# Optimization experiments

Hardware: AMD Instinct MI355X
Metric: run time of the kernel (lower is better)

The kernel has to match this reference:

```python
import jax, jax.numpy as jnp
import numpy as np

N_NODES = 50000
N_EDGES = 800000
EPS = 1e-5

def _xavier(key, shape):
    fan_in, fan_out = shape[1], shape[0]
    lim = float(np.sqrt(6.0 / (fan_in + fan_out)))
    return jax.random.uniform(key, shape, jnp.float32, -lim, lim)

def setup_inputs() -> dict:
    key = jax.random.key(0)
    ks = jax.random.split(key, 12)
    x = jax.random.normal(ks[0], (N_NODES, 166), jnp.float32)
    edge_index = jax.random.randint(ks[1], (2, N_EDGES), 0, N_NODES, jnp.int32)
    dims = [(256, 166), (128, 256), (64, 128)]
    inp = {"x": x, "edge_index": edge_index}
    # SAGEConv layers: lin_l (applied to aggregated neighbors, has bias) and lin_r (self)
    names = ["1", "2", "e"]
    for i, (nm, (do, di)) in enumerate(zip(names, dims)):
        inp[f"Wl{nm}"] = _xavier(ks[2 + 2 * i], (do, di))
        inp[f"Wr{nm}"] = _xavier(ks[3 + 2 * i], (do, di))
        inp[f"b{nm}"] = jnp.zeros((do,), jnp.float32)
    # BatchNorm params for the two hidden conv layers
    inp["g1"] = jnp.ones((256,), jnp.float32); inp["bt1"] = jnp.zeros((256,), jnp.float32)
    inp["g2"] = jnp.ones((128,), jnp.float32); inp["bt2"] = jnp.zeros((128,), jnp.float32)
    # classifier
    inp["Wc"] = _xavier(ks[8], (2, 64))
    inp["bc"] = jnp.zeros((2,), jnp.float32)
    return inp

def _sage_conv(x, src, dst, Wl, Wr, b):
    # mean aggregation of source features at destination nodes
    agg = jax.ops.segment_sum(x[src], dst, num_segments=N_NODES)  # [N, d]
    deg = jax.ops.segment_sum(jnp.ones((src.shape[0],), x.dtype), dst, num_segments=N_NODES)
    agg = agg / jnp.maximum(deg, 1.0)[:, None]
    return agg @ Wl.T + x @ Wr.T + b

def _bn(x, g, b):
    m = jnp.mean(x, axis=0)
    v = jnp.var(x, axis=0)
    return (x - m) * jax.lax.rsqrt(v + EPS) * g + b

def reference(x, edge_index, Wl1, Wr1, b1, Wl2, Wr2, b2, Wle, Wre, be, g1, bt1, g2, bt2, Wc, bc):
    src, dst = edge_index[0], edge_index[1]
    h = _sage_conv(x, src, dst, Wl1, Wr1, b1)
    h = jax.nn.relu(_bn(h, g1, bt1))
    h = _sage_conv(h, src, dst, Wl2, Wr2, b2)
    h = jax.nn.relu(_bn(h, g2, bt2))
    embeddings = _sage_conv(h, src, dst, Wle, Wre, be)  # [N, 64]
    logits = embeddings @ Wc.T + bc  # [N, 2]
    return (logits, embeddings)
```

## Files before the change

kernel.cpp:

```cpp
#include <hip/hip_runtime.h>

#define NN 50000
#define NE 800000
#define NB 256
#define BNODES ((NN + NB - 1) / NB)
#define CAP 4096
static constexpr float BN_EPS = 1e-5f;

typedef __attribute__((ext_vector_type(8))) short bf16x8;
typedef __attribute__((ext_vector_type(4))) float f32x4;

__device__ inline unsigned short f2bf(float f) {
  unsigned int u = __float_as_uint(f);
  return (unsigned short)((u + 0x7FFFu + ((u >> 16) & 1u)) >> 16);
}
__device__ inline float bf2f(unsigned int h) { return __uint_as_float(h << 16); }
__device__ inline void gl_lds16(const char* g, char* l) {
  __builtin_amdgcn_global_load_lds((const __attribute__((address_space(1))) void*)g,
                                   (__attribute__((address_space(3))) void*)l, 16, 0, 0);
}

__global__ void k_bpart(const int* __restrict__ src, const int* __restrict__ dst,
                        int* __restrict__ bcur, uint2* __restrict__ pairs) {
  __shared__ int cnt[NB], lbase[NB], lcur[NB];
  int t = threadIdx.x;
  cnt[t] = 0;
  __syncthreads();
  int e0 = blockIdx.x * 8192 + t;
#pragma unroll
  for (int i = 0; i < 32; ++i) {
    int e = e0 + i * 256;
    if (e < NE) atomicAdd(&cnt[dst[e] / BNODES], 1);
  }
  __syncthreads();
  lbase[t] = cnt[t] ? (t * CAP + atomicAdd(&bcur[t], cnt[t])) : 0;
  lcur[t] = 0;
  __syncthreads();
#pragma unroll
  for (int i = 0; i < 32; ++i) {
    int e = e0 + i * 256;
    if (e < NE) {
      int d = dst[e];
      int b = d / BNODES;
      int p = atomicAdd(&lcur[b], 1);
      pairs[(size_t)lbase[b] + p] = uint2{(unsigned)src[e], (unsigned)d};
    }
  }
}

__global__ void k_bscatter(const uint2* __restrict__ pairs, const int* __restrict__ bcur,
                           int2* __restrict__ begend, int* __restrict__ col) {
  __shared__ int dcnt[NB], ts[NB], doff[NB], dcur[NB];
  int t = threadIdx.x;
  int b = blockIdx.x;
  int n0 = b * BNODES;
  int ncnt = min(NN - n0, BNODES);
  int e0 = b * CAP, e1 = e0 + bcur[b];
  dcnt[t] = 0;
  __syncthreads();
  for (int e = e0 + t; e < e1; e += 256) atomicAdd(&dcnt[pairs[e].y - n0], 1);
  __syncthreads();
  ts[t] = dcnt[t];
  __syncthreads();
#pragma unroll
  for (int off = 1; off < NB; off <<= 1) {
    int u = (t >= off) ? ts[t - off] : 0;
    __syncthreads();
    ts[t] += u;
    __syncthreads();
  }
  doff[t] = ts[t] - dcnt[t];
  dcur[t] = 0;
  if (t < ncnt) begend[n0 + t] = int2{e0 + doff[t], e0 + doff[t] + dcnt[t]};
  __syncthreads();
  for (int e = e0 + t; e < e1; e += 256) {
    uint2 pr = pairs[e];
    int ld = pr.y - n0;
    int p = atomicAdd(&dcur[ld], 1);
    col[e0 + doff[ld] + p] = (int)pr.x;
  }
}

__global__ void k_prep_x(const float* __restrict__ x, unsigned int* __restrict__ xbu,
                         unsigned int* __restrict__ X1u) {
  int i = blockIdx.x * 256 + threadIdx.x;
  if (i >= NN * 96) return;
  int r = i / 96, q = i - r * 96;
  if (q < 84) {
    int c0 = 2 * q, c1 = c0 + 1;
    float v0 = (c0 < 166) ? x[(size_t)r * 166 + c0] : 0.f;
    float v1 = (c1 < 166) ? x[(size_t)r * 166 + c1] : 0.f;
    unsigned int u = (unsigned)f2bf(v0) | ((unsigned)f2bf(v1) << 16);
    xbu[(size_t)r * 96 + q] = u;
    X1u[(size_t)r * 192 + 96 + q] = u;
  } else {
    int z = q - 84;
    X1u[(size_t)r * 192 + 84 + z] = 0u;
    X1u[(size_t)r * 192 + 180 + z] = 0u;
    if (z == 0) X1u[(size_t)r * 192 + 83] = 0u;
  }
}

__global__ void k_pack_w_all(const float* __restrict__ Wl1, const float* __restrict__ Wr1,
                             const float* __restrict__ Wl2, const float* __restrict__ Wr2,
                             const float* __restrict__ Wle, const float* __restrict__ Wre,
                             unsigned short* __restrict__ w1c, unsigned short* __restrict__ w2s,
                             unsigned short* __restrict__ w3s) {
  int idx = blockIdx.x * 256 + threadIdx.x;
  if (idx < 98304) {
    int n = idx / 384, k = idx - n * 384;
    float v = 0.f;
    if (k < 166) v = Wl1[(size_t)n * 166 + k];
    else if (k >= 192 && k < 358) v = Wr1[(size_t)n * 166 + (k - 192)];
    w1c[idx] = f2bf(v);
  } else if (idx < 163840) {
    int j = idx - 98304;
    int n = j / 256, k = j - n * 256;
    w2s[j] = f2bf(n < 128 ? Wl2[(size_t)n * 256 + k] : Wr2[(size_t)(n - 128) * 256 + k]);
  } else if (idx < 180224) {
    int j = idx - 163840;
    int n = j / 128, k = j - n * 128;
    w3s[j] = f2bf(n < 64 ? Wle[(size_t)n * 128 + k] : Wre[(size_t)(n - 64) * 128 + k]);
  }
}

template <int D, int U, bool FUSE, bool OUTBF, bool CLS>
__global__ __launch_bounds__(256) void k_aggb(
    const unsigned int* __restrict__ feat, int fsu,
    const int2* __restrict__ begend, const int* __restrict__ col,
    const unsigned int* __restrict__ self, int ssu,
    const float* __restrict__ bias,
    void* __restrict__ outv, int osu,
    const float* __restrict__ Wc, const float* __restrict__ bc,
    float* __restrict__ logits) {
  constexpr int D2 = D / 2;
  constexpr int LPN = (D2 < 64) ? D2 : 64;
  constexpr int NPB = 256 / LPN;
  constexpr int C = (D2 + LPN - 1) / LPN;
  int node = blockIdx.x * NPB + threadIdx.x / LPN;
  if (node >= NN) return;
  int lane = threadIdx.x % LPN;
  int2 be = begend[node];
  int beg = be.x, end = be.y;
  float ax[C], ay[C];
#pragma unroll
  for (int c = 0; c < C; ++c) { ax[c] = 0.f; ay[c] = 0.f; }

  int j = beg;
  for (; j + U <= end; j += U) {
    const unsigned int* fp[U];
#pragma unroll
    for (int u = 0; u < U; ++u) fp[u] = feat + (size_t)col[j + u] * fsu;
#pragma unroll
    for (int c = 0; c < C; ++c) {
      int p = lane + c * LPN;
      unsigned int t[U];
#pragma unroll
      for (int u = 0; u < U; ++u) t[u] = (p < D2) ? fp[u][p] : 0u;
#pragma unroll
      for (int u = 0; u < U; ++u) {
        ax[c] += bf2f(t[u] & 0xffffu);
        ay[c] += bf2f(t[u] >> 16);
      }
    }
  }
  for (; j < end; ++j) {
    const unsigned int* fr = feat + (size_t)col[j] * fsu;
#pragma unroll
    for (int c = 0; c < C; ++c) {
      int p = lane + c * LPN;
      if (p < D2) {
        unsigned int t = fr[p];
        ax[c] += bf2f(t & 0xffffu);
        ay[c] += bf2f(t >> 16);
      }
    }
  }
  float inv = 1.0f / fmaxf((float)(end - beg), 1.0f);
  float s0 = 0.f, s1 = 0.f;
#pragma unroll
  for (int c = 0; c < C; ++c) {
    int p = lane + c * LPN;
    if (p < D2) {
      float vx = ax[c] * inv, vy = ay[c] * inv;
      if constexpr (FUSE) {
        unsigned int s = self[(size_t)node * ssu + p];
        vx += bf2f(s & 0xffffu) + bias[2 * p];
        vy += bf2f(s >> 16) + bias[2 * p + 1];
      }
      if constexpr (OUTBF) {
        unsigned int o = (unsigned int)f2bf(vx) | ((unsigned int)f2bf(vy) << 16);
        ((unsigned int*)outv)[(size_t)node * osu + p] = o;
      } else {
        float2 o{vx, vy};
        *reinterpret_cast<float2*>((float*)outv + (size_t)node * osu + 2 * p) = o;
      }
      if constexpr (CLS) {
        s0 += vx * Wc[2 * p] + vy * Wc[2 * p + 1];
        s1 += vx * Wc[64 + 2 * p] + vy * Wc[64 + 2 * p + 1];
      }
    }
  }
  if constexpr (CLS) {
#pragma unroll
    for (int m = 1; m < LPN; m <<= 1) {
      s0 += __shfl_xor(s0, m);
      s1 += __shfl_xor(s1, m);
    }
    if (lane == 0) {
      logits[node * 2 + 0] = s0 + bc[0];
      logits[node * 2 + 1] = s1 + bc[1];
    }
  }
}

template <bool BIASED, bool STATS>
__global__ __launch_bounds__(256) void k_gemm_mfma(
    const unsigned short* __restrict__ A, int KC,
    const unsigned short* __restrict__ W,
    const float* __restrict__ bias,
    unsigned short* __restrict__ out, int Ntot,
    float* __restrict__ statacc) {
  __shared__ __align__(16) char lds[65536];
  int tid = threadIdx.x;
  int lane = tid & 63;
  int w = tid >> 6;
  int wr = w >> 1, wc = w & 1;
  int m0 = blockIdx.x * 128;
  int n0 = blockIdx.y * 128;

  int srow = lane >> 3;
  int scol = (lane & 7) << 4;
  int ssw = scol ^ (srow << 4);
  const char* Ab = (const char*)A;
  const char* Wb = (const char*)W;

  f32x4 acc[4][4];
#pragma unroll
  for (int i = 0; i < 4; ++i)
#pragma unroll
    for (int j = 0; j < 4; ++j) acc[i][j] = f32x4{0.f, 0.f, 0.f, 0.f};

  auto stage = [&](int buf, int k0) {
    char* dst = lds + buf * 32768 + w * 4096;
#pragma unroll
    for (int i = 0; i < 4; ++i) {
      int row = w * 32 + i * 8 + srow;
      int ga = m0 + row;
      ga = ga < NN ? ga : NN - 1;
      gl_lds16(Ab + ((size_t)ga * KC + k0) * 2 + ssw, dst + i * 1024);
      gl_lds16(Wb + ((size_t)(n0 + row) * KC + k0) * 2 + ssw, dst + 16384 + i * 1024);
    }
  };
  auto compute = [&](int buf) {
    char* lA = lds + buf * 32768;
    char* lB = lA + 16384;
#pragma unroll
    for (int ks = 0; ks < 2; ++ks) {
      bf16x8 af[4], bfr[4];
      int ac = ks * 64 + ((lane >> 4) << 4);
#pragma unroll
      for (int f = 0; f < 4; ++f) {
        int ar = wr * 64 + f * 16 + (lane & 15);
        af[f] = *reinterpret_cast<const bf16x8*>(lA + ar * 128 + (ac ^ ((ar & 7) << 4)));
        int br = wc * 64 + f * 16 + (lane & 15);
        bfr[f] = *reinterpret_cast<const bf16x8*>(lB + br * 128 + (ac ^ ((br & 7) << 4)));
      }
#pragma unroll
      for (int fm = 0; fm < 4; ++fm)
#pragma unroll
        for (int fn = 0; fn < 4; ++fn)
          acc[fm][fn] = __builtin_amdgcn_mfma_f32_16x16x32_bf16(af[fm], bfr[fn], acc[fm][fn], 0, 0, 0);
    }
  };

  int nt = KC >> 6;
  stage(0, 0);
  __syncthreads();
  int cur = 0;
  for (int t = 0; t < nt; ++t) {
    if (t + 1 < nt) stage(cur ^ 1, (t + 1) << 6);
    compute(cur);
    __syncthreads();
    cur ^= 1;
  }

  int nbase = n0 + wc * 64 + (lane & 15);
  float bv[4] = {0.f, 0.f, 0.f, 0.f};
  if constexpr (BIASED) {
#pragma unroll
    for (int fn = 0; fn < 4; ++fn) bv[fn] = bias[nbase + fn * 16];
  }
  float ssum[4] = {0.f, 0.f, 0.f, 0.f}, sqs[4] = {0.f, 0.f, 0.f, 0.f};
#pragma unroll
  for (int fm = 0; fm < 4; ++fm) {
    int mbase = m0 + wr * 64 + fm * 16 + ((lane >> 4) << 2);
#pragma unroll
    for (int j = 0; j < 4; ++j) {
      int m = mbase + j;
      if (m < NN) {
#pragma unroll
        for (int fn = 0; fn < 4; ++fn) {
          float v = acc[fm][fn][j] + bv[fn];
          out[(size_t)m * Ntot + nbase + fn * 16] = f2bf(v);
          if constexpr (STATS) { ssum[fn] += v; sqs[fn] += v * v; }
        }
      }
    }
  }
  if constexpr (STATS) {
#pragma unroll
    for (int fn = 0; fn < 4; ++fn) {
      float s = ssum[fn], q = sqs[fn];
      s += __shfl_xor(s, 16); s += __shfl_xor(s, 32);
      q += __shfl_xor(q, 16); q += __shfl_xor(q, 32);
      if (lane < 16) {
        atomicAdd(&statacc[nbase + fn * 16], s);
        atomicAdd(&statacc[Ntot + nbase + fn * 16], q);
      }
    }
  }
}

template <int N, bool BF>
__global__ __launch_bounds__(256) void k_bn_stats2(const void* __restrict__ hv,
                                                   float* __restrict__ acc) {
  constexpr int CP = N / 2;
  constexpr int RG = 256 / CP;
  int cp = threadIdx.x % CP, rg = threadIdx.x / CP;
  int rpb = (NN + gridDim.x - 1) / gridDim.x;
  int r0 = blockIdx.x * rpb, r1 = min(r0 + rpb, NN);
  float s0 = 0.f, s1 = 0.f, q0 = 0.f, q1 = 0.f;
  for (int r = r0 + rg; r < r1; r += RG) {
    float v0, v1;
    if constexpr (BF) {
      unsigned int u = ((const unsigned int*)hv)[(size_t)r * CP + cp];
      v0 = bf2f(u & 0xffffu); v1 = bf2f(u >> 16);
    } else {
      float2 u = ((const float2*)hv)[(size_t)r * CP + cp];
      v0 = u.x; v1 = u.y;
    }
    s0 += v0; s1 += v1; q0 += v0 * v0; q1 += v1 * v1;
  }
  __shared__ float l0[256], l1[256], l2[256], l3[256];
  l0[threadIdx.x] = s0; l1[threadIdx.x] = s1; l2[threadIdx.x] = q0; l3[threadIdx.x] = q1;
  __syncthreads();
  if (rg == 0) {
#pragma unroll
    for (int g = 1; g < RG; ++g) {
      s0 += l0[g * CP + cp]; s1 += l1[g * CP + cp];
      q0 += l2[g * CP + cp]; q1 += l3[g * CP + cp];
    }
    atomicAdd(&acc[2 * cp], s0);
    atomicAdd(&acc[2 * cp + 1], s1);
    atomicAdd(&acc[N + 2 * cp], q0);
    atomicAdd(&acc[N + 2 * cp + 1], q1);
  }
}

template <int N, bool INF32>
__global__ void k_bn_apply2(const void* __restrict__ hv, const float* __restrict__ acc,
                            const float* __restrict__ g, const float* __restrict__ b,
                            unsigned int* __restrict__ out) {
  constexpr int N2 = N / 2;
  int p = blockIdx.x * 256 + threadIdx.x;
  if (p >= NN * N2) return;
  int cp = p % N2;
  int c0 = 2 * cp, c1 = c0 + 1;
  float v0, v1;
  if constexpr (INF32) {
    float2 u = reinterpret_cast<const float2*>(hv)[p];
    v0 = u.x; v1 = u.y;
  } else {
    unsigned int u = reinterpret_cast<const unsigned int*>(hv)[p];
    v0 = bf2f(u & 0xffffu); v1 = bf2f(u >> 16);
  }
  float m0 = acc[c0] * (1.0f / NN);
  float m1 = acc[c1] * (1.0f / NN);
  float sc0 = g[c0] * rsqrtf(acc[N + c0] * (1.0f / NN) - m0 * m0 + BN_EPS);
  float sc1 = g[c1] * rsqrtf(acc[N + c1] * (1.0f / NN) - m1 * m1 + BN_EPS);
  float r0 = fmaxf((v0 - m0) * sc0 + b[c0], 0.f);
  float r1 = fmaxf((v1 - m1) * sc1 + b[c1], 0.f);
  out[p] = (unsigned int)f2bf(r0) | ((unsigned int)f2bf(r1) << 16);
}

extern "C" void kernel_launch(void* const* d_in, const int* in_sizes, int n_in,
                              void* d_out, int out_size, void* d_ws, size_t ws_size,
                              hipStream_t stream) {
  const float* x   = (const float*)d_in[0];
  const int* ei    = (const int*)d_in[1];
  const float* Wl1 = (const float*)d_in[2];
  const float* Wr1 = (const float*)d_in[3];
  const float* b1  = (const float*)d_in[4];
  const float* Wl2 = (const float*)d_in[5];
  const float* Wr2 = (const float*)d_in[6];
  const float* b2  = (const float*)d_in[7];
  const float* Wle = (const float*)d_in[8];
  const float* Wre = (const float*)d_in[9];
  const float* be  = (const float*)d_in[10];
  const float* g1  = (const float*)d_in[11];
  const float* bt1 = (const float*)d_in[12];
  const float* g2  = (const float*)d_in[13];
  const float* bt2 = (const float*)d_in[14];
  const float* Wc  = (const float*)d_in[15];
  const float* bc  = (const float*)d_in[16];

  const int* src = ei;
  const int* dst = ei + NE;

  char* ws = (char*)d_ws;
  size_t off = 0;
  auto take = [&](size_t bytes) -> char* {
    char* p = ws + off;
    off = (off + bytes + 255) & ~(size_t)255;
    return p;
  };
  int* bkt_cur   = (int*)take(1024);
  float* bnacc1  = (float*)take(2048);
  float* bnacc2  = (float*)take(2048);
  int2* begend   = (int2*)take((size_t)NN * 8);
  uint2* pairs   = (uint2*)take((size_t)NB * CAP * 8);
  int* col       = (int*)take((size_t)NB * CAP * 4);
  unsigned short* w1c = (unsigned short*)take((size_t)256 * 384 * 2);
  unsigned short* w2s = (unsigned short*)take((size_t)256 * 256 * 2);
  unsigned short* w3s = (unsigned short*)take((size_t)128 * 128 * 2);
  unsigned int* xbu = (unsigned int*)take((size_t)NN * 96 * 4);
  char* P0 = take((size_t)NN * 384 * 2);
  char* P1 = take((size_t)NN * 256 * 2);

  unsigned short* XC1   = (unsigned short*)P0;
  unsigned short* h1raw = (unsigned short*)P1;
  unsigned short* h1    = (unsigned short*)P0;
  unsigned short* z2    = (unsigned short*)P1;
  float*          h2raw = (float*)P0;
  unsigned short* h2    = (unsigned short*)P1;
  unsigned short* z3    = (unsigned short*)P0;

  float* logits = (float*)d_out;
  float* emb    = (float*)d_out + (size_t)NN * 2;

  hipMemsetAsync(bkt_cur, 0, 5120, stream);

  k_bpart<<<(NE + 8191) / 8192, 256, 0, stream>>>(src, dst, bkt_cur, pairs);
  k_bscatter<<<NB, NB, 0, stream>>>(pairs, bkt_cur, begend, col);

  k_prep_x<<<(NN * 96 + 255) / 256, 256, 0, stream>>>(x, xbu, (unsigned int*)XC1);
  k_pack_w_all<<<(180224 + 255) / 256, 256, 0, stream>>>(Wl1, Wr1, Wl2, Wr2, Wle, Wre, w1c, w2s, w3s);

  k_aggb<166, 4, false, true, false><<<(NN + 3) / 4, 256, 0, stream>>>(
      xbu, 96, begend, col, nullptr, 0, nullptr, (unsigned int*)XC1, 192,
      nullptr, nullptr, nullptr);
  {
    dim3 g((NN + 127) / 128, 2);
    k_gemm_mfma<true, true><<<g, 256, 0, stream>>>(XC1, 384, w1c, b1, h1raw, 256, bnacc1);
  }
  k_bn_apply2<256, false><<<(NN * 128 + 255) / 256, 256, 0, stream>>>(
      h1raw, bnacc1, g1, bt1, (unsigned int*)h1);

  {
    dim3 g((NN + 127) / 128, 2);
    k_gemm_mfma<false, false><<<g, 256, 0, stream>>>(h1, 256, w2s, nullptr, z2, 256, nullptr);
  }
  k_aggb<128, 8, true, false, false><<<(NN + 3) / 4, 256, 0, stream>>>(
      (const unsigned int*)z2, 128, begend, col, (const unsigned int*)z2 + 64, 128, b2,
      h2raw, 128, nullptr, nullptr, nullptr);
  k_bn_stats2<128, false><<<512, 256, 0, stream>>>(h2raw, bnacc2);
  k_bn_apply2<128, true><<<(NN * 64 + 255) / 256, 256, 0, stream>>>(
      h2raw, bnacc2, g2, bt2, (unsigned int*)h2);

  {
    dim3 g((NN + 127) / 128, 1);
    k_gemm_mfma<false, false><<<g, 256, 0, stream>>>(h2, 128, w3s, nullptr, z3, 128, nullptr);
  }
  k_aggb<64, 8, true, false, true><<<(NN + 7) / 8, 256, 0, stream>>>(
      (const unsigned int*)z3, 64, begend, col, (const unsigned int*)z3 + 32, 64, be,
      emb, 64, Wc, bc, logits);
}
```

Baseline: 309.4 us.

## Merge front-end prep kernels and read GEMM1 operands from two separate buffers

Combines the edge bucketing, x-to-bf16 conversion, weight packing and BN-accumulator zeroing into one launch with block-range dispatch, removing several kernel launches and shrinking the memset. The first GEMM now takes two A pointers (aggregated features and self features) selected per K-chunk, so the concatenated XC1 buffer no longer has to be built and the duplicate write of x into it is gone. The trade-off is a per-stage pointer select in the GEMM and a mixed-role kernel whose partitions have uneven cost.

```diff
diff --git a/kernel.cpp b/kernel.cpp
--- a/kernel.cpp
+++ b/kernel.cpp
@@ -5,6 +5,9 @@
 #define NB 256
 #define BNODES ((NN + NB - 1) / NB)
 #define CAP 4096
+#define BPART_BLKS ((NE + 8191) / 8192)
+#define PREP_BLKS ((NN * 112 + 255) / 256)
+#define PACK_BLKS ((180224 + 255) / 256)
 static constexpr float BN_EPS = 1e-5f;
 
 typedef __attribute__((ext_vector_type(8))) short bf16x8;
@@ -20,13 +23,13 @@
                                    (__attribute__((address_space(3))) void*)l, 16, 0, 0);
 }
 
-__global__ void k_bpart(const int* __restrict__ src, const int* __restrict__ dst,
-                        int* __restrict__ bcur, uint2* __restrict__ pairs) {
+__device__ void dev_bpart(int bb, const int* __restrict__ src, const int* __restrict__ dst,
+                          int* __restrict__ bcur, uint2* __restrict__ pairs) {
   __shared__ int cnt[NB], lbase[NB], lcur[NB];
   int t = threadIdx.x;
   cnt[t] = 0;
   __syncthreads();
-  int e0 = blockIdx.x * 8192 + t;
+  int e0 = bb * 8192 + t;
 #pragma unroll
   for (int i = 0; i < 32; ++i) {
     int e = e0 + i * 256;
@@ -46,6 +49,62 @@
       pairs[(size_t)lbase[b] + p] = uint2{(unsigned)src[e], (unsigned)d};
     }
   }
+}
+
+__global__ void k_front(const int* __restrict__ src, const int* __restrict__ dst,
+                        int* __restrict__ bcur, uint2* __restrict__ pairs,
+                        const float* __restrict__ x, unsigned int* __restrict__ xbu,
+                        unsigned int* __restrict__ aggX,
+                        const float* __restrict__ Wl1, const float* __restrict__ Wr1,
+                        const float* __restrict__ Wl2, const float* __restrict__ Wr2,
+                        const float* __restrict__ Wle, const float* __restrict__ Wre,
+                        unsigned short* __restrict__ w1c, unsigned short* __restrict__ w2s,
+                        unsigned short* __restrict__ w3s,
+                        float* __restrict__ bnacc) {
+  int b = blockIdx.x;
+  if (b < BPART_BLKS) {
+    dev_bpart(b, src, dst, bcur, pairs);
+    return;
+  }
+  b -= BPART_BLKS;
+  if (b < PREP_BLKS) {
+    int i = b * 256 + threadIdx.x;
+    if (i >= NN * 112) return;
+    int r = i / 112, q = i - r * 112;
+    if (q < 84) {
+      int c0 = 2 * q, c1 = c0 + 1;
+      float v0 = (c0 < 166) ? x[(size_t)r * 166 + c0] : 0.f;
+      float v1 = (c1 < 166) ? x[(size_t)r * 166 + c1] : 0.f;
+      xbu[(size_t)r * 96 + q] = (unsigned)f2bf(v0) | ((unsigned)f2bf(v1) << 16);
+    } else if (q < 96) {
+      xbu[(size_t)r * 96 + q] = 0u;
+    } else if (q < 109) {
+      aggX[(size_t)r * 96 + 83 + (q - 96)] = 0u;
+    }
+    return;
+  }
+  b -= PREP_BLKS;
+  if (b < PACK_BLKS) {
+    int idx = b * 256 + threadIdx.x;
+    if (idx < 98304) {
+      int n = idx / 384, k = idx - n * 384;
+      float v = 0.f;
+      if (k < 166) v = Wl1[(size_t)n * 166 + k];
+      else if (k >= 192 && k < 358) v = Wr1[(size_t)n * 166 + (k - 192)];
+      w1c[idx] = f2bf(v);
+    } else if (idx < 163840) {
+      int j = idx - 98304;
+      int n = j / 256, k = j - n * 256;
+      w2s[j] = f2bf(n < 128 ? Wl2[(size_t)n * 256 + k] : Wr2[(size_t)(n - 128) * 256 + k]);
+    } else if (idx < 180224) {
+      int j = idx - 163840;
+      int n = j / 128, k = j - n * 128;
+      w3s[j] = f2bf(n < 64 ? Wle[(size_t)n * 128 + k] : Wre[(size_t)(n - 64) * 128 + k]);
+    }
+    return;
+  }
+  int z = (b - PACK_BLKS) * 256 + threadIdx.x;
+  if (z < 1024) bnacc[z] = 0.f;
 }
 
 __global__ void k_bscatter(const uint2* __restrict__ pairs, const int* __restrict__ bcur,
@@ -78,49 +137,6 @@
     int ld = pr.y - n0;
     int p = atomicAdd(&dcur[ld], 1);
     col[e0 + doff[ld] + p] = (int)pr.x;
-  }
-}
-
-__global__ void k_prep_x(const float* __restrict__ x, unsigned int* __restrict__ xbu,
-                         unsigned int* __restrict__ X1u) {
-  int i = blockIdx.x * 256 + threadIdx.x;
-  if (i >= NN * 96) return;
-  int r = i / 96, q = i - r * 96;
-  if (q < 84) {
-    int c0 = 2 * q, c1 = c0 + 1;
-    float v0 = (c0 < 166) ? x[(size_t)r * 166 + c0] : 0.f;
-    float v1 = (c1 < 166) ? x[(size_t)r * 166 + c1] : 0.f;
-    unsigned int u = (unsigned)f2bf(v0) | ((unsigned)f2bf(v1) << 16);
-    xbu[(size_t)r * 96 + q] = u;
-    X1u[(size_t)r * 192 + 96 + q] = u;
-  } else {
-    int z = q - 84;
-    X1u[(size_t)r * 192 + 84 + z] = 0u;
-    X1u[(size_t)r * 192 + 180 + z] = 0u;
-    if (z == 0) X1u[(size_t)r * 192 + 83] = 0u;
-  }
-}
-
-__global__ void k_pack_w_all(const float* __restrict__ Wl1, const float* __restrict__ Wr1,
-                             const float* __restrict__ Wl2, const float* __restrict__ Wr2,
-                             const float* __restrict__ Wle, const float* __restrict__ Wre,
-                             unsigned short* __restrict__ w1c, unsigned short* __restrict__ w2s,
-                             unsigned short* __restrict__ w3s) {
-  int idx = blockIdx.x * 256 + threadIdx.x;
-  if (idx < 98304) {
-    int n = idx / 384, k = idx - n * 384;
-    float v = 0.f;
-    if (k < 166) v = Wl1[(size_t)n * 166 + k];
-    else if (k >= 192 && k < 358) v = Wr1[(size_t)n * 166 + (k - 192)];
-    w1c[idx] = f2bf(v);
-  } else if (idx < 163840) {
-    int j = idx - 98304;
-    int n = j / 256, k = j - n * 256;
-    w2s[j] = f2bf(n < 128 ? Wl2[(size_t)n * 256 + k] : Wr2[(size_t)(n - 128) * 256 + k]);
-  } else if (idx < 180224) {
-    int j = idx - 163840;
-    int n = j / 128, k = j - n * 128;
-    w3s[j] = f2bf(n < 64 ? Wle[(size_t)n * 128 + k] : Wre[(size_t)(n - 64) * 128 + k]);
   }
 }
 
@@ -216,7 +232,8 @@
 
 template <bool BIASED, bool STATS>
 __global__ __launch_bounds__(256) void k_gemm_mfma(
-    const unsigned short* __restrict__ A, int KC,
+    const unsigned short* __restrict__ A0, const unsigned short* __restrict__ A1,
+    int K1, int Astride, int KC,
     const unsigned short* __restrict__ W,
     const float* __restrict__ bias,
     unsigned short* __restrict__ out, int Ntot,
@@ -232,7 +249,6 @@
   int srow = lane >> 3;
   int scol = (lane & 7) << 4;
   int ssw = scol ^ (srow << 4);
-  const char* Ab = (const char*)A;
   const char* Wb = (const char*)W;
 
   f32x4 acc[4][4];
@@ -242,13 +258,15 @@
     for (int j = 0; j < 4; ++j) acc[i][j] = f32x4{0.f, 0.f, 0.f, 0.f};
 
   auto stage = [&](int buf, int k0) {
+    const char* Ab = (const char*)(k0 < K1 ? A0 : A1);
+    int koff = k0 < K1 ? k0 : k0 - K1;
     char* dst = lds + buf * 32768 + w * 4096;
 #pragma unroll
     for (int i = 0; i < 4; ++i) {
       int row = w * 32 + i * 8 + srow;
       int ga = m0 + row;
       ga = ga < NN ? ga : NN - 1;
-      gl_lds16(Ab + ((size_t)ga * KC + k0) * 2 + ssw, dst + i * 1024);
+      gl_lds16(Ab + ((size_t)ga * Astride + koff) * 2 + ssw, dst + i * 1024);
       gl_lds16(Wb + ((size_t)(n0 + row) * KC + k0) * 2 + ssw, dst + 16384 + i * 1024);
     }
   };
@@ -424,11 +442,11 @@
   unsigned short* w1c = (unsigned short*)take((size_t)256 * 384 * 2);
   unsigned short* w2s = (unsigned short*)take((size_t)256 * 256 * 2);
   unsigned short* w3s = (unsigned short*)take((size_t)128 * 128 * 2);
-  unsigned int* xbu = (unsigned int*)take((size_t)NN * 96 * 4);
-  char* P0 = take((size_t)NN * 384 * 2);
+  unsigned int* xbu  = (unsigned int*)take((size_t)NN * 96 * 4);
+  unsigned int* aggX = (unsigned int*)take((size_t)NN * 96 * 4);
   char* P1 = take((size_t)NN * 256 * 2);
-
-  unsigned short* XC1   = (unsigned short*)P0;
+  char* P0 = take((size_t)NN * 256 * 2);
+
   unsigned short* h1raw = (unsigned short*)P1;
   unsigned short* h1    = (unsigned short*)P0;
   unsigned short* z2    = (unsigned short*)P1;
@@ -439,27 +457,30 @@
   float* logits = (float*)d_out;
   float* emb    = (float*)d_out + (size_t)NN * 2;
 
-  hipMemsetAsync(bkt_cur, 0, 5120, stream);
-
-  k_bpart<<<(NE + 8191) / 8192, 256, 0, stream>>>(src, dst, bkt_cur, pairs);
+  hipMemsetAsync(bkt_cur, 0, 1024, stream);
+
+  {
+    int grid = BPART_BLKS + PREP_BLKS + PACK_BLKS + 4;
+    k_front<<<grid, 256, 0, stream>>>(src, dst, bkt_cur, pairs, x, xbu, aggX,
+                                      Wl1, Wr1, Wl2, Wr2, Wle, Wre, w1c, w2s, w3s, bnacc1);
+  }
   k_bscatter<<<NB, NB, 0, stream>>>(pairs, bkt_cur, begend, col);
 
-  k_prep_x<<<(NN * 96 + 255) / 256, 256, 0, stream>>>(x, xbu, (unsigned int*)XC1);
-  k_pack_w_all<<<(180224 + 255) / 256, 256, 0, stream>>>(Wl1, Wr1, Wl2, Wr2, Wle, Wre, w1c, w2s, w3s);
-
   k_aggb<166, 4, false, true, false><<<(NN + 3) / 4, 256, 0, stream>>>(
-      xbu, 96, begend, col, nullptr, 0, nullptr, (unsigned int*)XC1, 192,
-      nullptr, nullptr, nullptr);
+      xbu, 96, begend, col, nullptr, 0, nullptr, aggX, 96, nullptr, nullptr, nullptr);
   {
     dim3 g((NN + 127) / 128, 2);
-    k_gemm_mfma<true, true><<<g, 256, 0, stream>>>(XC1, 384, w1c, b1, h1raw, 256, bnacc1);
+    k_gemm_mfma<true, true><<<g, 256, 0, stream>>>(
+        (const unsigned short*)aggX, (const unsigned short*)xbu, 192, 192, 384,
+        w1c, b1, h1raw, 256, bnacc1);
   }
   k_bn_apply2<256, false><<<(NN * 128 + 255) / 256, 256, 0, stream>>>(
       h1raw, bnacc1, g1, bt1, (unsigned int*)h1);
 
   {
     dim3 g((NN + 127) / 128, 2);
-    k_gemm_mfma<false, false><<<g, 256, 0, stream>>>(h1, 256, w2s, nullptr, z2, 256, nullptr);
+    k_gemm_mfma<false, false><<<g, 256, 0, stream>>>(
+        h1, h1, 1 << 30, 256, 256, w2s, nullptr, z2, 256, nullptr);
   }
   k_aggb<128, 8, true, false, false><<<(NN + 3) / 4, 256, 0, stream>>>(
       (const unsigned int*)z2, 128, begend, col, (const unsigned int*)z2 + 64, 128, b2,
@@ -470,7 +491,8 @@
 
   {
     dim3 g((NN + 127) / 128, 1);
-    k_gemm_mfma<false, false><<<g, 256, 0, stream>>>(h2, 128, w3s, nullptr, z3, 128, nullptr);
+    k_gemm_mfma<false, false><<<g, 256, 0, stream>>>(
+        h2, h2, 1 << 30, 128, 128, w3s, nullptr, z3, 128, nullptr);
   }
   k_aggb<64, 8, true, false, true><<<(NN + 7) / 8, 256, 0, stream>>>(
       (const unsigned int*)z3, 64, begend, col, (const unsigned int*)z3 + 32, 64, be,
```

New measurement: 291.6 us. 1.06x faster.
